# Kernel tuning notes

Measured on AMD Instinct MI355X. Metric: run time of the kernel, lower is better.

## Reference

```python
import jax, jax.numpy as jnp
import numpy as np

H = 16
D_MODEL = 1024
HEAD_DIM = D_MODEL // H
NEG = -1e9


def setup_inputs() -> dict:
    key = jax.random.key(0)
    k1, k2, k3, k4, k5, k6 = jax.random.split(key, 6)
    B, L = 2, 2048
    feature = jax.random.normal(k1, (B, L, D_MODEL), dtype=jnp.float32)
    mask = jax.random.randint(k2, (B, L), 0, 2, dtype=jnp.int32)
    # Linear weights stored torch-style as [out, in]; biases zero-init per initialize().
    s = 1.0 / np.sqrt(D_MODEL)
    W_Q = jax.random.uniform(k3, (D_MODEL, D_MODEL), jnp.float32, -s, s)
    W_K = jax.random.uniform(k4, (D_MODEL, D_MODEL), jnp.float32, -s, s)
    W_V = jax.random.uniform(k5, (D_MODEL, D_MODEL), jnp.float32, -s, s)
    b_Q = jnp.zeros((D_MODEL,), jnp.float32)
    b_K = jnp.zeros((D_MODEL,), jnp.float32)
    b_V = jnp.zeros((D_MODEL,), jnp.float32)
    return {"feature": feature, "mask": mask, "W_Q": W_Q, "b_Q": b_Q,
            "W_K": W_K, "b_K": b_K, "W_V": W_V, "b_V": b_V}


def reference(feature, mask, W_Q, b_Q, W_K, b_K, W_V, b_V):
    B, L, _ = feature.shape
    scale = jnp.sqrt(jnp.float32(HEAD_DIM))
    # Projections: torch Linear is x @ W^T + b. Split into heads: [B, H, L, Dh]
    def proj(W, b):
        y = feature @ W.T + b
        return y.reshape(B, L, H, HEAD_DIM).transpose(0, 2, 1, 3)
    Q = proj(W_Q, b_Q)
    K = proj(W_K, b_K)
    V = proj(W_V, b_V)
    # Scores [B, H, Lq, Lk]
    A = jnp.einsum('bhqd,bhkd->bhqk', Q, K) / scale
    # Key-side mask broadcast over heads and query positions
    A = jnp.where(mask[:, None, None, :] == 0, jnp.float32(NEG), A)
    alpha = jax.nn.softmax(A, axis=-1)
    out = jnp.einsum('bhqk,bhkd->bhqd', alpha, V)  # [B, H, L, Dh]
    return out.transpose(0, 2, 1, 3).reshape(B, L, H * HEAD_DIM)
```

## Files before the change

### kernel.cpp

```cpp
#include <hip/hip_runtime.h>

typedef __bf16 bf16;
typedef __attribute__((ext_vector_type(4))) __bf16 bf16x4;
typedef __attribute__((ext_vector_type(8))) __bf16 bf16x8;
typedef __attribute__((ext_vector_type(4))) float f32x4;
typedef __attribute__((ext_vector_type(16))) float f32x16;
typedef unsigned int u32;

#define D_MODEL 1024
#define SEQ_L   2048
#define NHEAD   16
#define HDIM    64
#define MROWS   4096

#define S_SCALE 0.18033688f

#define FEAT_OFF  512u
#define WQ_OFF    (FEAT_OFF + 4194304u)
#define WK_OFF    (WQ_OFF + 1048576u)
#define WV_OFF    (WK_OFF + 1048576u)
#define BQ_OFF    (WV_OFF + 1048576u)
#define BK_OFF    (BQ_OFF + 1024u)
#define BV_OFF    (BK_OFF + 1024u)
#define Q_OFF     (BV_OFF + 1024u)
#define K_OFF     (Q_OFF + 4194304u)
#define V_OFF     (K_OFF + 4194304u)

typedef const __attribute__((address_space(1))) u32* gp_t;
typedef __attribute__((address_space(3))) u32* lp_t;
__device__ __forceinline__ void ld16(const bf16* g, bf16* l) {
    __builtin_amdgcn_global_load_lds((gp_t)g, (lp_t)l, 16, 0, 0);
}

__global__ void convert_in(const float* __restrict__ feat,
                           const float* __restrict__ wq, const float* __restrict__ wk,
                           const float* __restrict__ wv,
                           const float* __restrict__ bq, const float* __restrict__ bk,
                           const float* __restrict__ bv,
                           bf16* __restrict__ ws) {
    const int bid = blockIdx.x;
    const float* src; bf16* dst; int off; float sc = 1.0f;
    if (bid < 4096)      { src = feat; dst = ws + FEAT_OFF; off = bid * 1024; }
    else if (bid < 5120) { src = wq;   dst = ws + WQ_OFF;   off = (bid - 4096) * 1024; sc = S_SCALE; }
    else if (bid < 6144) { src = wk;   dst = ws + WK_OFF;   off = (bid - 5120) * 1024; }
    else if (bid < 7168) { src = wv;   dst = ws + WV_OFF;   off = (bid - 6144) * 1024; }
    else if (bid == 7168){ src = bq;   dst = ws + BQ_OFF;   off = 0; sc = S_SCALE; }
    else if (bid == 7169){ src = bk;   dst = ws + BK_OFF;   off = 0; }
    else                 { src = bv;   dst = ws + BV_OFF;   off = 0; }
    int idx = off + threadIdx.x * 4;
    float4 v = *(const float4*)(src + idx);
    bf16x4 o;
    o[0] = (bf16)(v.x * sc);
    o[1] = (bf16)(v.y * sc);
    o[2] = (bf16)(v.z * sc);
    o[3] = (bf16)(v.w * sc);
    *(bf16x4*)(dst + idx) = o;
}

__global__ __launch_bounds__(256, 2) void qkv_gemm(const bf16* __restrict__ ws,
                                                   bf16* __restrict__ wsw,
                                                   const int* __restrict__ mask) {
    __shared__ bf16 smem[3 * 128 * 64];
    bf16* Alds = smem;
    bf16* B0   = smem + 8192;
    bf16* B1   = smem + 16384;

    const int zi   = blockIdx.z;
    const int t    = threadIdx.x;
    const int lane = t & 63;
    const int wave = t >> 6;
    const int quad = lane >> 4;
    const int l16  = lane & 15;
    const int wrow = (wave >> 1) * 64;
    const int wcol = (wave & 1) * 64;
    const int r8 = lane >> 3;
    const int sl = lane & 7;
    const int sg = sl ^ r8;

    if (zi == 0) {
        const bf16* X   = ws + FEAT_OFF;
        const bf16* Wq  = ws + WQ_OFF;
        const bf16* Wk  = ws + WK_OFF;
        const int m0 = blockIdx.x * 128;
        const int n0 = blockIdx.y * 128;

        f32x4 aq[4][4], ak[4][4];
        for (int mi = 0; mi < 4; ++mi)
            for (int ni = 0; ni < 4; ++ni) {
                aq[mi][ni] = (f32x4){0.f, 0.f, 0.f, 0.f};
                ak[mi][ni] = (f32x4){0.f, 0.f, 0.f, 0.f};
            }

        for (int k0 = 0; k0 < D_MODEL; k0 += 64) {
#pragma unroll
            for (int i = 0; i < 4; ++i) {
                int ch  = wave * 4 + i;
                int row = ch * 8 + r8;
                ld16(X  + (size_t)(m0 + row) * D_MODEL + k0 + sg * 8, Alds + ch * 512);
                ld16(Wq + (size_t)(n0 + row) * D_MODEL + k0 + sg * 8, B0   + ch * 512);
                ld16(Wk + (size_t)(n0 + row) * D_MODEL + k0 + sg * 8, B1   + ch * 512);
            }
            __syncthreads();

#pragma unroll
            for (int kk = 0; kk < 2; ++kk) {
                const int sgb = quad + kk * 4;
                bf16x8 af[4];
#pragma unroll
                for (int mi = 0; mi < 4; ++mi) {
                    int row = wrow + mi * 16 + l16;
                    af[mi] = *(const bf16x8*)(&Alds[row * 64 + ((sgb ^ (row & 7)) << 3)]);
                }
                {
                    bf16x8 bfr[4];
#pragma unroll
                    for (int ni = 0; ni < 4; ++ni) {
                        int row = wcol + ni * 16 + l16;
                        bfr[ni] = *(const bf16x8*)(&B0[row * 64 + ((sgb ^ (row & 7)) << 3)]);
                    }
#pragma unroll
                    for (int mi = 0; mi < 4; ++mi)
#pragma unroll
                        for (int ni = 0; ni < 4; ++ni)
                            aq[mi][ni] = __builtin_amdgcn_mfma_f32_16x16x32_bf16(
                                af[mi], bfr[ni], aq[mi][ni], 0, 0, 0);
                }
                {
                    bf16x8 bfr[4];
#pragma unroll
                    for (int ni = 0; ni < 4; ++ni) {
                        int row = wcol + ni * 16 + l16;
                        bfr[ni] = *(const bf16x8*)(&B1[row * 64 + ((sgb ^ (row & 7)) << 3)]);
                    }
#pragma unroll
                    for (int mi = 0; mi < 4; ++mi)
#pragma unroll
                        for (int ni = 0; ni < 4; ++ni)
                            ak[mi][ni] = __builtin_amdgcn_mfma_f32_16x16x32_bf16(
                                af[mi], bfr[ni], ak[mi][ni], 0, 0, 0);
                }
            }
            __syncthreads();
        }

        bf16* Yq = wsw + Q_OFF;
        bf16* Yk = wsw + K_OFF;
        const bf16* bq = ws + BQ_OFF;
        const bf16* bk = ws + BK_OFF;
#pragma unroll
        for (int ni = 0; ni < 4; ++ni) {
            int col = n0 + wcol + ni * 16 + l16;
            float bqf = (float)bq[col];
            float bkf = (float)bk[col];
#pragma unroll
            for (int mi = 0; mi < 4; ++mi) {
                int rowb = m0 + wrow + mi * 16 + quad * 4;
#pragma unroll
                for (int r = 0; r < 4; ++r) {
                    Yq[(size_t)(rowb + r) * D_MODEL + col] = (bf16)(aq[mi][ni][r] + bqf);
                    float v = ak[mi][ni][r] + bkf;
                    if (mask[rowb + r] == 0) v = 0.f;
                    Yk[(size_t)(rowb + r) * D_MODEL + col] = (bf16)v;
                }
            }
        }
    } else {
        const bf16* Amat = ws + WV_OFF;
        const bf16* Bmat = ws + FEAT_OFF;
        const bf16* bias = ws + BV_OFF;
        bf16* Y = wsw + V_OFF;
        const int m0 = blockIdx.y * 128;
        const int n0 = blockIdx.x * 128;

        f32x4 acc[4][4];
        for (int mi = 0; mi < 4; ++mi)
            for (int ni = 0; ni < 4; ++ni)
                acc[mi][ni] = (f32x4){0.f, 0.f, 0.f, 0.f};

        for (int k0 = 0; k0 < D_MODEL; k0 += 64) {
#pragma unroll
            for (int i = 0; i < 4; ++i) {
                int ch  = wave * 4 + i;
                int row = ch * 8 + r8;
                ld16(Amat + (size_t)(m0 + row) * D_MODEL + k0 + sg * 8, Alds + ch * 512);
                ld16(Bmat + (size_t)(n0 + row) * D_MODEL + k0 + sg * 8, B0   + ch * 512);
            }
            __syncthreads();

#pragma unroll
            for (int kk = 0; kk < 2; ++kk) {
                const int sgb = quad + kk * 4;
                bf16x8 af[4], bfr[4];
#pragma unroll
                for (int mi = 0; mi < 4; ++mi) {
                    int row = wrow + mi * 16 + l16;
                    af[mi] = *(const bf16x8*)(&Alds[row * 64 + ((sgb ^ (row & 7)) << 3)]);
                }
#pragma unroll
                for (int ni = 0; ni < 4; ++ni) {
                    int row = wcol + ni * 16 + l16;
                    bfr[ni] = *(const bf16x8*)(&B0[row * 64 + ((sgb ^ (row & 7)) << 3)]);
                }
#pragma unroll
                for (int mi = 0; mi < 4; ++mi)
#pragma unroll
                    for (int ni = 0; ni < 4; ++ni)
                        acc[mi][ni] = __builtin_amdgcn_mfma_f32_16x16x32_bf16(
                            af[mi], bfr[ni], acc[mi][ni], 0, 0, 0);
            }
            __syncthreads();
        }

#pragma unroll
        for (int mi = 0; mi < 4; ++mi) {
#pragma unroll
            for (int r = 0; r < 4; ++r) {
                int rowv = m0 + wrow + mi * 16 + quad * 4 + r;
                float bvf = (float)bias[rowv];
#pragma unroll
                for (int ni = 0; ni < 4; ++ni) {
                    int col = n0 + wcol + ni * 16 + l16;
                    float v = acc[mi][ni][r] + bvf;
                    if (mask[col] == 0) v = 0.f;
                    size_t addr = (size_t)(col >> 11) * 2097152u +
                                  (size_t)rowv * 2048u + (col & 2047);
                    Y[addr] = (bf16)v;
                }
            }
        }
    }
}

__global__ __launch_bounds__(512, 4) void attn_kernel(
    const bf16* __restrict__ ws,
    const int* __restrict__ mask, float* __restrict__ out) {
    const int bh  = blockIdx.x;
    const int qt  = blockIdx.y;
    const int b   = bh >> 4, h = bh & 15;
    const int t    = threadIdx.x;
    const int lane = t & 63;
    const int wave = t >> 6;
    const int qh   = wave & 3;
    const int kh   = wave >> 2;
    const int half = lane >> 5;
    const int l31  = lane & 31;
    const int kt0  = kh * 1024;

    __shared__ bf16 smem[32768];
    bf16* Kb = smem;
    bf16* Vb = smem + 16384;

    const bf16* Qh  = ws + Q_OFF + (size_t)(b * SEQ_L) * D_MODEL + h * HDIM;
    const bf16* Kh  = ws + K_OFF + (size_t)(b * SEQ_L) * D_MODEL + h * HDIM;
    const bf16* Vth = ws + V_OFF + (size_t)b * 2097152u + (size_t)(h * HDIM) * SEQ_L;

    const int qrow0 = qt * 128 + qh * 32;
    bf16x8 qf[4];
#pragma unroll
    for (int ks = 0; ks < 4; ++ks)
        qf[ks] = *(const bf16x8*)(Qh + (size_t)(qrow0 + l31) * D_MODEL
                                  + ks * 16 + half * 8);

    bf16x8 ones;
#pragma unroll
    for (int j = 0; j < 8; ++j) ones[j] = (bf16)1.0f;

    f32x16 o[2], lacc;
    int nm = 0;
#pragma unroll
    for (int i = 0; i < 16; ++i) { o[0][i] = 0.f; o[1][i] = 0.f; lacc[i] = 0.f; }

    const int srow = (lane >> 3);
    const int sg   = (lane & 7) ^ srow;

#define STAGE(bb, kt)                                                          \
    do {                                                                       \
        _Pragma("unroll")                                                      \
        for (int i = 0; i < 2; ++i) {                                          \
            int row = i * 32 + qh * 8 + srow;                                  \
            ld16(Kh + (size_t)((kt) + row) * D_MODEL + sg * 8,                 \
                 Kb + (kh * 2 + (bb)) * 4096 + i * 2048 + qh * 512);           \
            ld16(Vth + (size_t)row * SEQ_L + (kt) + sg * 8,                    \
                 Vb + (kh * 2 + (bb)) * 4096 + i * 2048 + qh * 512);           \
        }                                                                      \
    } while (0)

    STAGE(0, kt0);
    __syncthreads();

    int cur = 0;
    for (int it = 0; it < 16; ++it) {
        const int kt = kt0 + it * 64;
        if (it < 15) STAGE(cur ^ 1, kt + 64);

        int mv = mask[b * SEQ_L + kt + lane];
        nm += (int)__popcll(__ballot(mv != 0));

        const bf16* Kcur = Kb + (kh * 2 + cur) * 4096;
        f32x16 st[2];
#pragma unroll
        for (int ktile = 0; ktile < 2; ++ktile) {
#pragma unroll
            for (int i = 0; i < 16; ++i) st[ktile][i] = 0.f;
#pragma unroll
            for (int ks = 0; ks < 4; ++ks) {
                const int row  = ktile * 32 + l31;
                const int slot = (ks * 2 + half) ^ (l31 & 7);
                bf16x8 kf = *(const bf16x8*)(&Kcur[row * 64 + slot * 8]);
                st[ktile] = __builtin_amdgcn_mfma_f32_32x32x16_bf16(
                    kf, qf[ks], st[ktile], 0, 0, 0);
            }
        }

        bf16x4 pk[2][4];
#pragma unroll
        for (int ktile = 0; ktile < 2; ++ktile) {
#pragma unroll
            for (int g = 0; g < 4; ++g) {
                bf16x4 pkv;
#pragma unroll
                for (int j = 0; j < 4; ++j)
                    pkv[j] = (bf16)__builtin_amdgcn_exp2f(st[ktile][g * 4 + j]);
                pk[ktile][g] = pkv;
            }
        }

        bf16x8 pf[4];
#pragma unroll
        for (int ks = 0; ks < 4; ++ks) {
            const int k1 = ks & 1, kt2 = ks >> 1;
            uint2 a  = __builtin_bit_cast(uint2, pk[kt2][2 * k1]);
            uint2 bb = __builtin_bit_cast(uint2, pk[kt2][2 * k1 + 1]);
            uint2 keep, send;
            keep.x = half ? bb.x : a.x;  keep.y = half ? bb.y : a.y;
            send.x = half ? a.x : bb.x;  send.y = half ? a.y : bb.y;
            uint2 recv;
            recv.x = (unsigned)__shfl_xor((int)send.x, 32);
            recv.y = (unsigned)__shfl_xor((int)send.y, 32);
            uint4 frag;
            frag.x = half ? recv.x : keep.x;
            frag.y = half ? recv.y : keep.y;
            frag.z = half ? keep.x : recv.x;
            frag.w = half ? keep.y : recv.y;
            pf[ks] = __builtin_bit_cast(bf16x8, frag);
        }

        const bf16* Vcur = Vb + (kh * 2 + cur) * 4096;
#pragma unroll
        for (int ks = 0; ks < 4; ++ks)
            lacc = __builtin_amdgcn_mfma_f32_32x32x16_bf16(pf[ks], ones, lacc, 0, 0, 0);
#pragma unroll
        for (int dt = 0; dt < 2; ++dt) {
#pragma unroll
            for (int ks = 0; ks < 4; ++ks) {
                const int row  = dt * 32 + l31;
                const int slot = (ks * 2 + half) ^ (l31 & 7);
                bf16x8 vf = *(const bf16x8*)(&Vcur[row * 64 + slot * 8]);
                o[dt] = __builtin_amdgcn_mfma_f32_32x32x16_bf16(
                    pf[ks], vf, o[dt], 0, 0, 0);
            }
        }

        __syncthreads();
        cur ^= 1;
    }
#undef STAGE

    const float corr = (float)(1024 - nm);
    float* ex = (float*)smem;
    const int slot = qh * 64 + lane;
    if (kh == 1) {
#pragma unroll
        for (int r = 0; r < 16; ++r) {
            ex[r * 256 + slot]        = o[0][r];
            ex[(16 + r) * 256 + slot] = o[1][r];
            ex[(32 + r) * 256 + slot] = lacc[r] - corr;
        }
    }
    __syncthreads();
    if (kh == 0) {
#pragma unroll
        for (int r = 0; r < 16; ++r) {
            const int q32 = (r & 3) + 8 * (r >> 2) + 4 * half;
            const int q = qrow0 + q32;
            const size_t base = ((size_t)(b * SEQ_L + q)) * D_MODEL + h * HDIM;
            const float l  = (lacc[r] - corr) + ex[(32 + r) * 256 + slot];
            const float rl = 1.0f / fmaxf(l, 1e-30f);
            out[base + l31]      = (o[0][r] + ex[r * 256 + slot]) * rl;
            out[base + 32 + l31] = (o[1][r] + ex[(16 + r) * 256 + slot]) * rl;
        }
    }
}

extern "C" void kernel_launch(void* const* d_in, const int* in_sizes, int n_in,
                              void* d_out, int out_size, void* d_ws, size_t ws_size,
                              hipStream_t stream) {
    const float* feat = (const float*)d_in[0];
    const int*   mask = (const int*)d_in[1];
    const float* Wq = (const float*)d_in[2];
    const float* bq = (const float*)d_in[3];
    const float* Wk = (const float*)d_in[4];
    const float* bk = (const float*)d_in[5];
    const float* Wv = (const float*)d_in[6];
    const float* bv = (const float*)d_in[7];

    bf16* ws = (bf16*)d_ws;

    convert_in<<<7171, 256, 0, stream>>>(feat, Wq, Wk, Wv, bq, bk, bv, ws);

    dim3 g1(32, 8, 2);
    qkv_gemm<<<g1, 256, 0, stream>>>(ws, ws, mask);

    dim3 g2(2 * NHEAD, SEQ_L / 128);
    attn_kernel<<<g2, 512, 0, stream>>>(ws, mask, (float*)d_out);
}
```

Baseline: 161.2 us.

## Double-buffer LDS staging in QKV GEMM to overlap loads with MFMA

Both QKV GEMM paths now prefetch the next K-tile into a second LDS buffer while computing on the current one, so each iteration needs one barrier instead of two. The QK path shrinks its K-step from 64 to 32 with a new swizzle so three double-buffered operands fit in 64KB of LDS. The V path keeps K-step 64 with two double-buffered operands. This hides global-to-LDS latency behind compute. The cost is more LDS per block, which may limit occupancy to fewer blocks per CU, and twice as many loop iterations in the QK path.

New measurement: 161.4 us. Within noise of the previous version (+0.1%).

```diff
diff --git a/kernel.cpp b/kernel.cpp
--- a/kernel.cpp
+++ b/kernel.cpp
@@ -60,11 +60,7 @@
 __global__ __launch_bounds__(256, 2) void qkv_gemm(const bf16* __restrict__ ws,
                                                    bf16* __restrict__ wsw,
                                                    const int* __restrict__ mask) {
-    __shared__ bf16 smem[3 * 128 * 64];
-    bf16* Alds = smem;
-    bf16* B0   = smem + 8192;
-    bf16* B1   = smem + 16384;
-
+    __shared__ bf16 smem[32768];
     const int zi   = blockIdx.z;
     const int t    = threadIdx.x;
     const int lane = t & 63;
@@ -73,17 +69,20 @@
     const int l16  = lane & 15;
     const int wrow = (wave >> 1) * 64;
     const int wcol = (wave & 1) * 64;
-    const int r8 = lane >> 3;
-    const int sl = lane & 7;
-    const int sg = sl ^ r8;
 
     if (zi == 0) {
+        bf16* Ab = smem;
+        bf16* Bq = smem + 8192;
+        bf16* Bk = smem + 16384;
         const bf16* X   = ws + FEAT_OFF;
         const bf16* Wq  = ws + WQ_OFF;
         const bf16* Wk  = ws + WK_OFF;
         const int m0 = blockIdx.x * 128;
         const int n0 = blockIdx.y * 128;
 
+        const int r4  = lane >> 2;
+        const int sgq = (lane & 3) ^ ((lane >> 3) & 3);
+
         f32x4 aq[4][4], ak[4][4];
         for (int mi = 0; mi < 4; ++mi)
             for (int ni = 0; ni < 4; ++ni) {
@@ -91,57 +90,59 @@
                 ak[mi][ni] = (f32x4){0.f, 0.f, 0.f, 0.f};
             }
 
-        for (int k0 = 0; k0 < D_MODEL; k0 += 64) {
-#pragma unroll
-            for (int i = 0; i < 4; ++i) {
-                int ch  = wave * 4 + i;
-                int row = ch * 8 + r8;
-                ld16(X  + (size_t)(m0 + row) * D_MODEL + k0 + sg * 8, Alds + ch * 512);
-                ld16(Wq + (size_t)(n0 + row) * D_MODEL + k0 + sg * 8, B0   + ch * 512);
-                ld16(Wk + (size_t)(n0 + row) * D_MODEL + k0 + sg * 8, B1   + ch * 512);
-            }
+#define STAGEQK(bb, k0)                                                        \
+    do {                                                                       \
+        _Pragma("unroll")                                                      \
+        for (int i = 0; i < 2; ++i) {                                          \
+            int ch  = wave * 2 + i;                                            \
+            int row = ch * 16 + r4;                                            \
+            ld16(X  + (size_t)(m0 + row) * D_MODEL + (k0) + sgq * 8,           \
+                 Ab + (bb) * 4096 + ch * 512);                                 \
+            ld16(Wq + (size_t)(n0 + row) * D_MODEL + (k0) + sgq * 8,           \
+                 Bq + (bb) * 4096 + ch * 512);                                 \
+            ld16(Wk + (size_t)(n0 + row) * D_MODEL + (k0) + sgq * 8,           \
+                 Bk + (bb) * 4096 + ch * 512);                                 \
+        }                                                                      \
+    } while (0)
+
+        STAGEQK(0, 0);
+        __syncthreads();
+
+        int cur = 0;
+        for (int k0 = 0; k0 < D_MODEL; k0 += 32) {
+            if (k0 + 32 < D_MODEL) STAGEQK(cur ^ 1, k0 + 32);
+
+            bf16x8 af[4], bq8[4], bk8[4];
+#pragma unroll
+            for (int mi = 0; mi < 4; ++mi) {
+                int row  = wrow + mi * 16 + l16;
+                int phys = quad ^ ((row >> 1) & 3);
+                af[mi] = *(const bf16x8*)(&Ab[cur * 4096 + row * 32 + phys * 8]);
+            }
+#pragma unroll
+            for (int ni = 0; ni < 4; ++ni) {
+                int row  = wcol + ni * 16 + l16;
+                int phys = quad ^ ((row >> 1) & 3);
+                bq8[ni] = *(const bf16x8*)(&Bq[cur * 4096 + row * 32 + phys * 8]);
+                bk8[ni] = *(const bf16x8*)(&Bk[cur * 4096 + row * 32 + phys * 8]);
+            }
+#pragma unroll
+            for (int mi = 0; mi < 4; ++mi)
+#pragma unroll
+                for (int ni = 0; ni < 4; ++ni)
+                    aq[mi][ni] = __builtin_amdgcn_mfma_f32_16x16x32_bf16(
+                        af[mi], bq8[ni], aq[mi][ni], 0, 0, 0);
+#pragma unroll
+            for (int mi = 0; mi < 4; ++mi)
+#pragma unroll
+                for (int ni = 0; ni < 4; ++ni)
+                    ak[mi][ni] = __builtin_amdgcn_mfma_f32_16x16x32_bf16(
+                        af[mi], bk8[ni], ak[mi][ni], 0, 0, 0);
+
             __syncthreads();
-
-#pragma unroll
-            for (int kk = 0; kk < 2; ++kk) {
-                const int sgb = quad + kk * 4;
-                bf16x8 af[4];
-#pragma unroll
-                for (int mi = 0; mi < 4; ++mi) {
-                    int row = wrow + mi * 16 + l16;
-                    af[mi] = *(const bf16x8*)(&Alds[row * 64 + ((sgb ^ (row & 7)) << 3)]);
-                }
-                {
-                    bf16x8 bfr[4];
-#pragma unroll
-                    for (int ni = 0; ni < 4; ++ni) {
-                        int row = wcol + ni * 16 + l16;
-                        bfr[ni] = *(const bf16x8*)(&B0[row * 64 + ((sgb ^ (row & 7)) << 3)]);
-                    }
-#pragma unroll
-                    for (int mi = 0; mi < 4; ++mi)
-#pragma unroll
-                        for (int ni = 0; ni < 4; ++ni)
-                            aq[mi][ni] = __builtin_amdgcn_mfma_f32_16x16x32_bf16(
-                                af[mi], bfr[ni], aq[mi][ni], 0, 0, 0);
-                }
-                {
-                    bf16x8 bfr[4];
-#pragma unroll
-                    for (int ni = 0; ni < 4; ++ni) {
-                        int row = wcol + ni * 16 + l16;
-                        bfr[ni] = *(const bf16x8*)(&B1[row * 64 + ((sgb ^ (row & 7)) << 3)]);
-                    }
-#pragma unroll
-                    for (int mi = 0; mi < 4; ++mi)
-#pragma unroll
-                        for (int ni = 0; ni < 4; ++ni)
-                            ak[mi][ni] = __builtin_amdgcn_mfma_f32_16x16x32_bf16(
-                                af[mi], bfr[ni], ak[mi][ni], 0, 0, 0);
-                }
-            }
-            __syncthreads();
-        }
+            cur ^= 1;
+        }
+#undef STAGEQK
 
         bf16* Yq = wsw + Q_OFF;
         bf16* Yk = wsw + K_OFF;
@@ -165,6 +166,8 @@
             }
         }
     } else {
+        bf16* Ab = smem;
+        bf16* Bb = smem + 16384;
         const bf16* Amat = ws + WV_OFF;
         const bf16* Bmat = ws + FEAT_OFF;
         const bf16* bias = ws + BV_OFF;
@@ -172,20 +175,34 @@
         const int m0 = blockIdx.y * 128;
         const int n0 = blockIdx.x * 128;
 
+        const int r8 = lane >> 3;
+        const int sl = lane & 7;
+        const int sg = sl ^ r8;
+
         f32x4 acc[4][4];
         for (int mi = 0; mi < 4; ++mi)
             for (int ni = 0; ni < 4; ++ni)
                 acc[mi][ni] = (f32x4){0.f, 0.f, 0.f, 0.f};
 
+#define STAGEV(bb, k0)                                                         \
+    do {                                                                       \
+        _Pragma("unroll")                                                      \
+        for (int i = 0; i < 4; ++i) {                                          \
+            int ch  = wave * 4 + i;                                            \
+            int row = ch * 8 + r8;                                             \
+            ld16(Amat + (size_t)(m0 + row) * D_MODEL + (k0) + sg * 8,          \
+                 Ab + (bb) * 8192 + ch * 512);                                 \
+            ld16(Bmat + (size_t)(n0 + row) * D_MODEL + (k0) + sg * 8,          \
+                 Bb + (bb) * 8192 + ch * 512);                                 \
+        }                                                                      \
+    } while (0)
+
+        STAGEV(0, 0);
+        __syncthreads();
+
+        int cur = 0;
         for (int k0 = 0; k0 < D_MODEL; k0 += 64) {
-#pragma unroll
-            for (int i = 0; i < 4; ++i) {
-                int ch  = wave * 4 + i;
-                int row = ch * 8 + r8;
-                ld16(Amat + (size_t)(m0 + row) * D_MODEL + k0 + sg * 8, Alds + ch * 512);
-                ld16(Bmat + (size_t)(n0 + row) * D_MODEL + k0 + sg * 8, B0   + ch * 512);
-            }
-            __syncthreads();
+            if (k0 + 64 < D_MODEL) STAGEV(cur ^ 1, k0 + 64);
 
 #pragma unroll
             for (int kk = 0; kk < 2; ++kk) {
@@ -194,12 +211,14 @@
 #pragma unroll
                 for (int mi = 0; mi < 4; ++mi) {
                     int row = wrow + mi * 16 + l16;
-                    af[mi] = *(const bf16x8*)(&Alds[row * 64 + ((sgb ^ (row & 7)) << 3)]);
+                    af[mi] = *(const bf16x8*)(
+                        &Ab[cur * 8192 + row * 64 + ((sgb ^ (row & 7)) << 3)]);
                 }
 #pragma unroll
                 for (int ni = 0; ni < 4; ++ni) {
                     int row = wcol + ni * 16 + l16;
-                    bfr[ni] = *(const bf16x8*)(&B0[row * 64 + ((sgb ^ (row & 7)) << 3)]);
+                    bfr[ni] = *(const bf16x8*)(
+                        &Bb[cur * 8192 + row * 64 + ((sgb ^ (row & 7)) << 3)]);
                 }
 #pragma unroll
                 for (int mi = 0; mi < 4; ++mi)
@@ -208,8 +227,11 @@
                         acc[mi][ni] = __builtin_amdgcn_mfma_f32_16x16x32_bf16(
                             af[mi], bfr[ni], acc[mi][ni], 0, 0, 0);
             }
+
             __syncthreads();
-        }
+            cur ^= 1;
+        }
+#undef STAGEV
 
 #pragma unroll
         for (int mi = 0; mi < 4; ++mi) {
```
